# Optimization experiments

Hardware: AMD Instinct MI355X
Metric: run time of the kernel (lower is better)

Reference implementation:

```python
import jax, jax.numpy as jnp
import numpy as np

# Geometry constants fixed by the source's index arithmetic
GRID_P, GRID_Q, NUM_ANCH = 60, 40, 9   # p = (i//9)%60, q = i//(60*9), sr = i%9
N = GRID_P * GRID_Q * NUM_ANCH          # 21600 anchors per image
K = 1000                                # top-K candidates kept before NMS
MAX_BOXES = 18                          # fixed output boxes per image
THRESH = 0.5                            # NMS overlap threshold
BATCH = 64


def setup_inputs() -> dict:
    key = jax.random.key(0)
    k1, k2 = jax.random.split(key)
    x = jax.random.normal(k1, (BATCH, N, 6), dtype=jnp.float32)
    # anchor boxes (x, y, w, h); keep w,h strictly positive and away from 0
    anchor_boxes = jax.random.uniform(k2, (GRID_P, GRID_Q, NUM_ANCH, 4),
                                      dtype=jnp.float32, minval=0.05, maxval=1.0)
    return {"x": x, "anchor_boxes": anchor_boxes}


def _per_sample(ypred, anchors):
    scores, order = jax.lax.top_k(ypred[:, 0], K)          # descending, matches tf.argsort DESC [:1000]
    p = (order // NUM_ANCH) % GRID_P
    q = order // (GRID_P * NUM_ANCH)
    sr = order % NUM_ANCH
    a = anchors[p, q, sr]                                   # [K, 4] (xa, ya, wa, ha)
    regr = ypred[order, 2:6]                                # [K, 4] (dx, dy, dw, dh)
    xc = regr[:, 0] * a[:, 2] + a[:, 0]
    yc = regr[:, 1] * a[:, 3] + a[:, 1]
    w = a[:, 2] * jnp.exp(regr[:, 2])
    h = a[:, 3] * jnp.exp(regr[:, 3])
    cand = jnp.stack([xc, yc, w, h, scores], axis=-1)       # [K, 5] xywh+score

    # xywh -> xyxy for overlap computation (as in non_max_suppression_fast)
    x1 = xc - 0.5 * w; x2 = xc + 0.5 * w
    y1 = yc - 0.5 * h; y2 = yc + 0.5 * h
    area = (x2 - x1) * (y2 - y1)                            # [K]

    # pairwise intersection; overlap[i, j] = inter(i, j) / area(j)  (source divides by
    # the area of the lower-scored candidate, NOT the union -- kept faithfully)
    xx1 = jnp.maximum(x1[:, None], x1[None, :])
    yy1 = jnp.maximum(y1[:, None], y1[None, :])
    xx2 = jnp.minimum(x2[:, None], x2[None, :])
    yy2 = jnp.minimum(y2[:, None], y2[None, :])
    iw = jnp.maximum(0.0, xx2 - xx1)
    ih = jnp.maximum(0.0, yy2 - yy1)
    sup = (iw * ih / area[None, :]) > THRESH                # [K, K] bool

    # greedy NMS over candidates in descending-score order
    jrange = jnp.arange(K)
    def body(i, keep):
        return keep & ~(keep[i] & sup[i] & (jrange > i))
    keep = jax.lax.fori_loop(0, K, body, jnp.ones((K,), dtype=bool))

    # pack first MAX_BOXES kept boxes into fixed-shape output
    ranks = jnp.cumsum(keep) - 1                            # position among kept
    valid = keep & (ranks < MAX_BOXES)
    picked = jnp.zeros((MAX_BOXES, 5), cand.dtype).at[
        jnp.where(valid, ranks, MAX_BOXES)
    ].set(jnp.where(valid[:, None], cand, 0.0), mode='drop')

    # pad with top-scored decoded boxes if fewer than MAX_BOXES survive NMS
    n = jnp.minimum(jnp.sum(keep), MAX_BOXES)
    j = jnp.arange(MAX_BOXES)
    pad = cand[jnp.clip(j - n, 0, K - 1)]
    return jnp.where((j < n)[:, None], picked, pad)         # [MAX_BOXES, 5]


def reference(x, anchor_boxes):
    return jax.vmap(lambda y: _per_sample(y, anchor_boxes))(x)  # [B, 18, 5]
```

## Files before the change

kernel.cpp:

```cpp
#include <hip/hip_runtime.h>

#define NELEM 21600
#define KSEL 1000
#define MAXB 18
#define NT 1024
#define CAP 2048
#define NFULL 21
#define NTAIL (NELEM - NFULL * NT)

typedef unsigned long long ull;

__device__ __forceinline__ unsigned fkey(float f) {
  unsigned u = __float_as_uint(f);
  return (u & 0x80000000u) ? ~u : (u | 0x80000000u);
}
__device__ __forceinline__ float unfkey(unsigned k) {
  unsigned u = (k & 0x80000000u) ? (k ^ 0x80000000u) : ~k;
  return __uint_as_float(u);
}

__device__ void select_bucket(const unsigned* hist, unsigned target,
                              volatile unsigned* chunkSuf,
                              unsigned* outB, unsigned* outCnt, unsigned* outAbove) {
  const int tid = threadIdx.x;
  const int w = tid >> 6, l = tid & 63;
  unsigned h1 = hist[w * 128 + 2 * l + 1];
  unsigned s = hist[w * 128 + 2 * l] + h1;
  #pragma unroll
  for (int d = 1; d < 64; d <<= 1) {
    unsigned t = __shfl_down(s, d);
    if (l + d < 64) s += t;
  }
  if (l == 0) chunkSuf[w] = s;
  __syncthreads();
  if (w == 0) {
    unsigned ct = (l < 16) ? chunkSuf[l] : 0u;
    unsigned cs = ct;
    #pragma unroll
    for (int d = 1; d < 16; d <<= 1) {
      unsigned t = __shfl_down(cs, d);
      if (l + d < 16) cs += t;
    }
    if (l < 16) chunkSuf[l] = cs - ct;
  }
  __syncthreads();
  unsigned base = chunkSuf[w];
  unsigned sufE = s + base;
  unsigned sN = __shfl_down(s, 1);
  unsigned sufN = ((l < 63) ? sN : 0u) + base;
  unsigned geOdd = sufN + h1;
  if (sufE >= target && geOdd < target) { *outB = w * 128u + 2u * l;     *outCnt = sufE;  *outAbove = geOdd; }
  if (geOdd >= target && sufN < target) { *outB = w * 128u + 2u * l + 1; *outCnt = geOdd; *outAbove = sufN;  }
  __syncthreads();
}

__global__ __launch_bounds__(NT, 4) void rpn_kernel(
    const float* __restrict__ x, const float* __restrict__ anch,
    float* __restrict__ out) {
  const int b = blockIdx.x;
  const int tid = threadIdx.x;
  const float* xb = x + (size_t)b * NELEM * 6;

  __shared__ unsigned hist[2048];
  __shared__ unsigned chunkSuf[16];
  __shared__ ull selPk[CAP];
  __shared__ float bX1[KSEL], bY1[KSEL], bX2[KSEL], bY2[KSEL], bAr[KSEL];
  __shared__ unsigned sB, sCnt, sAbove;
  __shared__ unsigned baseKey;
  __shared__ unsigned cnt;
  __shared__ int keptRank[MAXB];
  __shared__ int numKept;

  hist[2 * tid] = 0u; hist[2 * tid + 1] = 0u;

  float sv[NFULL];
  #pragma unroll
  for (int u = 0; u < NFULL; ++u)
    sv[u] = xb[(size_t)(tid + (u << 10)) * 6];
  float stail = 0.f;
  const bool hastail = tid < NTAIL;
  if (hastail) stail = xb[(size_t)(tid + NFULL * NT) * 6];
  asm volatile("" :
      "+v"(sv[0]), "+v"(sv[1]), "+v"(sv[2]), "+v"(sv[3]), "+v"(sv[4]),
      "+v"(sv[5]), "+v"(sv[6]), "+v"(sv[7]), "+v"(sv[8]), "+v"(sv[9]),
      "+v"(sv[10]), "+v"(sv[11]), "+v"(sv[12]), "+v"(sv[13]), "+v"(sv[14]),
      "+v"(sv[15]), "+v"(sv[16]), "+v"(sv[17]), "+v"(sv[18]), "+v"(sv[19]),
      "+v"(sv[20]), "+v"(stail));
  __syncthreads();

  #pragma unroll
  for (int u = 0; u < NFULL; ++u)
    atomicAdd(&hist[fkey(sv[u]) >> 21], 1u);
  if (hastail) atomicAdd(&hist[fkey(stail) >> 21], 1u);
  __syncthreads();
  select_bucket(hist, KSEL, chunkSuf, &sB, &sCnt, &sAbove);
  const unsigned b1 = sB, cnt1 = sCnt, above1 = sAbove;

  if (cnt1 <= CAP) {
    if (tid == 0) { baseKey = b1 << 21; cnt = 0u; }
  } else {
    hist[2 * tid] = 0u; hist[2 * tid + 1] = 0u;
    __syncthreads();
    #pragma unroll
    for (int u = 0; u < NFULL; ++u) {
      unsigned k = fkey(sv[u]);
      if ((k >> 21) == b1) atomicAdd(&hist[(k >> 10) & 0x7FFu], 1u);
    }
    if (hastail) {
      unsigned k = fkey(stail);
      if ((k >> 21) == b1) atomicAdd(&hist[(k >> 10) & 0x7FFu], 1u);
    }
    __syncthreads();
    select_bucket(hist, KSEL - above1, chunkSuf, &sB, &sCnt, &sAbove);
    if (tid == 0) { baseKey = (b1 << 21) | (sB << 10); cnt = 0u; }
  }
  __syncthreads();

  const unsigned TB = baseKey;
  #pragma unroll
  for (int u = 0; u < NFULL; ++u) {
    unsigned k = fkey(sv[u]);
    if (k >= TB) {
      unsigned p = atomicAdd(&cnt, 1u);
      unsigned i = (unsigned)(tid + (u << 10));
      if (p < CAP) selPk[p] = ((ull)k << 32) | (unsigned)(~i);
    }
  }
  if (hastail) {
    unsigned k = fkey(stail);
    if (k >= TB) {
      unsigned p = atomicAdd(&cnt, 1u);
      unsigned i = (unsigned)(tid + NFULL * NT);
      if (p < CAP) selPk[p] = ((ull)k << 32) | (unsigned)(~i);
    }
  }
  __syncthreads();
  const unsigned realCnt = (cnt < CAP) ? cnt : CAP;
  for (unsigned i = realCnt + tid; i < CAP; i += NT) selPk[i] = 0ull;
  __syncthreads();

  {
    const int w = tid >> 6, L = tid & 63;
    const int ea = (w << 7) | (L << 1);
    ull a = selPk[ea], bb = selPk[ea + 1];
    #pragma unroll
    for (unsigned k = 2; k <= 128; k <<= 1) {
      #pragma unroll
      for (unsigned j = k >> 1; j >= 2; j >>= 1) {
        bool up = ((ea & k) == 0);
        bool lower = ((ea & j) == 0);
        bool takeMax = (up == lower);
        ull oa = __shfl_xor(a, (int)(j >> 1));
        ull ob = __shfl_xor(bb, (int)(j >> 1));
        a  = takeMax ? (a  > oa ? a  : oa) : (a  < oa ? a  : oa);
        bb = takeMax ? (bb > ob ? bb : ob) : (bb < ob ? bb : ob);
      }
      bool up = ((ea & k) == 0);
      ull mx = a > bb ? a : bb, mn = a > bb ? bb : a;
      a = up ? mx : mn; bb = up ? mn : mx;
    }
    selPk[ea] = a; selPk[ea + 1] = bb;
    __syncthreads();
    for (unsigned k = 256; k <= 2048; k <<= 1) {
      for (unsigned j = k >> 1; j >= 128; j >>= 1) {
        unsigned p = (unsigned)tid;
        unsigned vi = ((p & ~(j - 1)) << 1) | (p & (j - 1));
        unsigned li = vi | j;
        ull av = selPk[vi], cv = selPk[li];
        bool doswap = ((vi & k) == 0) ? (av < cv) : (av > cv);
        if (doswap) { selPk[vi] = cv; selPk[li] = av; }
        __syncthreads();
      }
      a = selPk[ea]; bb = selPk[ea + 1];
      bool up = (((unsigned)(w << 7) & k) == 0);
      #pragma unroll
      for (unsigned j = 64; j >= 2; j >>= 1) {
        bool lower = ((ea & j) == 0);
        bool takeMax = (up == lower);
        ull oa = __shfl_xor(a, (int)(j >> 1));
        ull ob = __shfl_xor(bb, (int)(j >> 1));
        a  = takeMax ? (a  > oa ? a  : oa) : (a  < oa ? a  : oa);
        bb = takeMax ? (bb > ob ? bb : ob) : (bb < ob ? bb : ob);
      }
      ull mx = a > bb ? a : bb, mn = a > bb ? bb : a;
      a = up ? mx : mn; bb = up ? mn : mx;
      selPk[ea] = a; selPk[ea + 1] = bb;
      __syncthreads();
    }
  }

  if (tid < KSEL) {
    unsigned idx = ~(unsigned)selPk[tid];
    const float2* e2 = (const float2*)(xb + (size_t)idx * 6 + 2);
    float2 ra = e2[0], rb = e2[1];
    unsigned pp = (idx / 9u) % 60u;
    unsigned qq = idx / 540u;
    unsigned sr = idx % 9u;
    const float* ap = anch + (((pp * 40u + qq) * 9u + sr) * 4u);
    float ax = ap[0], ay = ap[1], aw = ap[2], ah = ap[3];
    float xc = ra.x * aw + ax;
    float yc = ra.y * ah + ay;
    float w = aw * expf(rb.x);
    float h = ah * expf(rb.y);
    float x1 = xc - 0.5f * w, x2 = xc + 0.5f * w;
    float y1 = yc - 0.5f * h, y2 = yc + 0.5f * h;
    bX1[tid] = x1; bY1[tid] = y1; bX2[tid] = x2; bY2[tid] = y2;
    bAr[tid] = (x2 - x1) * (y2 - y1);
  }
  __syncthreads();

  if (tid < 64) {
    const int lane = tid;
    int nk = 0;
    float kx1 = 0.f, ky1 = 0.f, kx2 = 0.f, ky2 = 0.f;
    int krank = -1;
    for (int base = 0; base < KSEL && nk < MAXB; base += 64) {
      int c = base + lane;
      bool alive = (c < KSEL);
      int cc = alive ? c : 0;
      float x1 = bX1[cc], y1 = bY1[cc], x2 = bX2[cc], y2 = bY2[cc], ar = bAr[cc];
      for (int i = 0; i < nk; ++i) {
        float px1 = __shfl(kx1, i), py1 = __shfl(ky1, i);
        float px2 = __shfl(kx2, i), py2 = __shfl(ky2, i);
        float iw = fmaxf(fminf(x2, px2) - fmaxf(x1, px1), 0.f);
        float ih = fmaxf(fminf(y2, py2) - fmaxf(y1, py1), 0.f);
        if (iw * ih / ar > 0.5f) alive = false;
      }
      unsigned long long m = __ballot(alive);
      while (m) {
        int i = __builtin_ctzll(m);
        float px1 = __shfl(x1, i), py1 = __shfl(y1, i);
        float px2 = __shfl(x2, i), py2 = __shfl(y2, i);
        if (lane == nk) { kx1 = px1; ky1 = py1; kx2 = px2; ky2 = py2; krank = base + i; }
        ++nk;
        if (nk >= MAXB) break;
        if (alive && lane != i) {
          float iw = fmaxf(fminf(x2, px2) - fmaxf(x1, px1), 0.f);
          float ih = fmaxf(fminf(y2, py2) - fmaxf(y1, py1), 0.f);
          if (iw * ih / ar > 0.5f) alive = false;
        }
        if (lane == i) alive = false;
        m = __ballot(alive);
      }
    }
    if (lane == 0) numKept = nk;
    if (lane < nk) keptRank[lane] = krank;
  }
  __syncthreads();

  const int n = numKept;
  if (tid < MAXB) {
    int j = tid;
    int r = (j < n) ? keptRank[j] : (j - n);
    ull pk = selPk[r];
    unsigned idx = ~(unsigned)pk;
    float sc = unfkey((unsigned)(pk >> 32));
    const float2* e2 = (const float2*)(xb + (size_t)idx * 6 + 2);
    float2 ra = e2[0], rb = e2[1];
    unsigned pp = (idx / 9u) % 60u;
    unsigned qq = idx / 540u;
    unsigned sr = idx % 9u;
    const float* ap = anch + (((pp * 40u + qq) * 9u + sr) * 4u);
    float ax = ap[0], ay = ap[1], aw = ap[2], ah = ap[3];
    float xc = ra.x * aw + ax;
    float yc = ra.y * ah + ay;
    float w = aw * expf(rb.x);
    float h = ah * expf(rb.y);
    float* o = out + b * (MAXB * 5) + j * 5;
    o[0] = xc; o[1] = yc; o[2] = w; o[3] = h; o[4] = sc;
  }
}

extern "C" void kernel_launch(void* const* d_in, const int* in_sizes, int n_in,
                              void* d_out, int out_size, void* d_ws, size_t ws_size,
                              hipStream_t stream) {
  const float* x = (const float*)d_in[0];
  const float* anch = (const float*)d_in[1];
  float* out = (float*)d_out;
  const int B = in_sizes[0] / (NELEM * 6);
  rpn_kernel<<<dim3(B), dim3(NT), 0, stream>>>(x, anch, out);
}
```

Baseline: 63.94 us.

## Split score scan and histogram into a wide pre-pass kernel over chunks

Adds a first kernel that runs four blocks per image. Each block reads a quarter of the objectness scores, converts them to sortable keys, writes the keys compactly to workspace and stores a partial 2048-bin histogram. The select/NMS kernel then sums the partial histograms and reads the contiguous keys instead of the strided 24-byte-stride scores. The aim is to spread the strided load and histogram work across more CUs than the 64 single-block-per-image launch uses. In exchange it adds a second launch plus a workspace round-trip for keys and histograms.

```diff
diff --git a/kernel.cpp b/kernel.cpp
--- a/kernel.cpp
+++ b/kernel.cpp
@@ -5,6 +5,8 @@
 #define MAXB 18
 #define NT 1024
 #define CAP 2048
+#define NCHUNK 4
+#define CHUNK (NELEM / NCHUNK)
 #define NFULL 21
 #define NTAIL (NELEM - NFULL * NT)
 
@@ -17,6 +19,42 @@
 __device__ __forceinline__ float unfkey(unsigned k) {
   unsigned u = (k & 0x80000000u) ? (k ^ 0x80000000u) : ~k;
   return __uint_as_float(u);
+}
+
+__global__ __launch_bounds__(NT) void k1_scan(
+    const float* __restrict__ x, unsigned* __restrict__ gkeys,
+    unsigned* __restrict__ ghist) {
+  const int blk = blockIdx.x;
+  const int s = blk / NCHUNK, c = blk % NCHUNK;
+  const int t = threadIdx.x;
+  const float* xb = x + (size_t)s * NELEM * 6;
+
+  __shared__ unsigned h[2048];
+  h[2 * t] = 0u; h[2 * t + 1] = 0u;
+  __syncthreads();
+
+  const int base = c * CHUNK;
+  unsigned key[6];
+  bool on[6];
+  #pragma unroll
+  for (int k = 0; k < 6; ++k) {
+    int o = t + (k << 10);
+    on[k] = o < CHUNK;
+    int e = base + (on[k] ? o : 0);
+    key[k] = fkey(xb[(size_t)e * 6]);
+  }
+  #pragma unroll
+  for (int k = 0; k < 6; ++k) {
+    if (on[k]) {
+      int e = base + t + (k << 10);
+      gkeys[(size_t)s * NELEM + e] = key[k];
+      atomicAdd(&h[key[k] >> 21], 1u);
+    }
+  }
+  __syncthreads();
+  unsigned* gh = ghist + (size_t)blk * 2048;
+  gh[2 * t] = h[2 * t];
+  gh[2 * t + 1] = h[2 * t + 1];
 }
 
 __device__ void select_bucket(const unsigned* hist, unsigned target,
@@ -54,12 +92,14 @@
   __syncthreads();
 }
 
-__global__ __launch_bounds__(NT, 4) void rpn_kernel(
+__global__ __launch_bounds__(NT, 4) void k2_select(
     const float* __restrict__ x, const float* __restrict__ anch,
+    const unsigned* __restrict__ gkeys, const unsigned* __restrict__ ghist,
     float* __restrict__ out) {
-  const int b = blockIdx.x;
+  const int s = blockIdx.x;
   const int tid = threadIdx.x;
-  const float* xb = x + (size_t)b * NELEM * 6;
+  const float* xb = x + (size_t)s * NELEM * 6;
+  const unsigned* ks = gkeys + (size_t)s * NELEM;
 
   __shared__ unsigned hist[2048];
   __shared__ unsigned chunkSuf[16];
@@ -71,27 +111,29 @@
   __shared__ int keptRank[MAXB];
   __shared__ int numKept;
 
-  hist[2 * tid] = 0u; hist[2 * tid + 1] = 0u;
-
-  float sv[NFULL];
-  #pragma unroll
-  for (int u = 0; u < NFULL; ++u)
-    sv[u] = xb[(size_t)(tid + (u << 10)) * 6];
-  float stail = 0.f;
+  unsigned kv[NFULL];
+  #pragma unroll
+  for (int u = 0; u < NFULL; ++u) kv[u] = ks[tid + (u << 10)];
+  unsigned ktail = 0u;
   const bool hastail = tid < NTAIL;
-  if (hastail) stail = xb[(size_t)(tid + NFULL * NT) * 6];
+  if (hastail) ktail = ks[tid + NFULL * NT];
   asm volatile("" :
-      "+v"(sv[0]), "+v"(sv[1]), "+v"(sv[2]), "+v"(sv[3]), "+v"(sv[4]),
-      "+v"(sv[5]), "+v"(sv[6]), "+v"(sv[7]), "+v"(sv[8]), "+v"(sv[9]),
-      "+v"(sv[10]), "+v"(sv[11]), "+v"(sv[12]), "+v"(sv[13]), "+v"(sv[14]),
-      "+v"(sv[15]), "+v"(sv[16]), "+v"(sv[17]), "+v"(sv[18]), "+v"(sv[19]),
-      "+v"(sv[20]), "+v"(stail));
-  __syncthreads();
-
-  #pragma unroll
-  for (int u = 0; u < NFULL; ++u)
-    atomicAdd(&hist[fkey(sv[u]) >> 21], 1u);
-  if (hastail) atomicAdd(&hist[fkey(stail) >> 21], 1u);
+      "+v"(kv[0]), "+v"(kv[1]), "+v"(kv[2]), "+v"(kv[3]), "+v"(kv[4]),
+      "+v"(kv[5]), "+v"(kv[6]), "+v"(kv[7]), "+v"(kv[8]), "+v"(kv[9]),
+      "+v"(kv[10]), "+v"(kv[11]), "+v"(kv[12]), "+v"(kv[13]), "+v"(kv[14]),
+      "+v"(kv[15]), "+v"(kv[16]), "+v"(kv[17]), "+v"(kv[18]), "+v"(kv[19]),
+      "+v"(kv[20]), "+v"(ktail));
+
+  {
+    unsigned h0 = 0, h1 = 0;
+    #pragma unroll
+    for (int c = 0; c < NCHUNK; ++c) {
+      const unsigned* gh = ghist + (size_t)(s * NCHUNK + c) * 2048;
+      h0 += gh[2 * tid];
+      h1 += gh[2 * tid + 1];
+    }
+    hist[2 * tid] = h0; hist[2 * tid + 1] = h1;
+  }
   __syncthreads();
   select_bucket(hist, KSEL, chunkSuf, &sB, &sCnt, &sAbove);
   const unsigned b1 = sB, cnt1 = sCnt, above1 = sAbove;
@@ -102,14 +144,9 @@
     hist[2 * tid] = 0u; hist[2 * tid + 1] = 0u;
     __syncthreads();
     #pragma unroll
-    for (int u = 0; u < NFULL; ++u) {
-      unsigned k = fkey(sv[u]);
-      if ((k >> 21) == b1) atomicAdd(&hist[(k >> 10) & 0x7FFu], 1u);
-    }
-    if (hastail) {
-      unsigned k = fkey(stail);
-      if ((k >> 21) == b1) atomicAdd(&hist[(k >> 10) & 0x7FFu], 1u);
-    }
+    for (int u = 0; u < NFULL; ++u)
+      if ((kv[u] >> 21) == b1) atomicAdd(&hist[(kv[u] >> 10) & 0x7FFu], 1u);
+    if (hastail && (ktail >> 21) == b1) atomicAdd(&hist[(ktail >> 10) & 0x7FFu], 1u);
     __syncthreads();
     select_bucket(hist, KSEL - above1, chunkSuf, &sB, &sCnt, &sAbove);
     if (tid == 0) { baseKey = (b1 << 21) | (sB << 10); cnt = 0u; }
@@ -119,20 +156,16 @@
   const unsigned TB = baseKey;
   #pragma unroll
   for (int u = 0; u < NFULL; ++u) {
-    unsigned k = fkey(sv[u]);
-    if (k >= TB) {
+    if (kv[u] >= TB) {
       unsigned p = atomicAdd(&cnt, 1u);
       unsigned i = (unsigned)(tid + (u << 10));
-      if (p < CAP) selPk[p] = ((ull)k << 32) | (unsigned)(~i);
-    }
-  }
-  if (hastail) {
-    unsigned k = fkey(stail);
-    if (k >= TB) {
-      unsigned p = atomicAdd(&cnt, 1u);
-      unsigned i = (unsigned)(tid + NFULL * NT);
-      if (p < CAP) selPk[p] = ((ull)k << 32) | (unsigned)(~i);
-    }
+      if (p < CAP) selPk[p] = ((ull)kv[u] << 32) | (unsigned)(~i);
+    }
+  }
+  if (hastail && ktail >= TB) {
+    unsigned p = atomicAdd(&cnt, 1u);
+    unsigned i = (unsigned)(tid + NFULL * NT);
+    if (p < CAP) selPk[p] = ((ull)ktail << 32) | (unsigned)(~i);
   }
   __syncthreads();
   const unsigned realCnt = (cnt < CAP) ? cnt : CAP;
@@ -266,7 +299,7 @@
     float yc = ra.y * ah + ay;
     float w = aw * expf(rb.x);
     float h = ah * expf(rb.y);
-    float* o = out + b * (MAXB * 5) + j * 5;
+    float* o = out + s * (MAXB * 5) + j * 5;
     o[0] = xc; o[1] = yc; o[2] = w; o[3] = h; o[4] = sc;
   }
 }
@@ -278,5 +311,8 @@
   const float* anch = (const float*)d_in[1];
   float* out = (float*)d_out;
   const int B = in_sizes[0] / (NELEM * 6);
-  rpn_kernel<<<dim3(B), dim3(NT), 0, stream>>>(x, anch, out);
-}
+  unsigned* ghist = (unsigned*)d_ws;
+  unsigned* gkeys = ghist + (size_t)B * NCHUNK * 2048;
+  k1_scan<<<dim3(B * NCHUNK), dim3(NT), 0, stream>>>(x, gkeys, ghist);
+  k2_select<<<dim3(B), dim3(NT), 0, stream>>>(x, anch, gkeys, ghist, out);
+}
```

New measurement: 65.66 us. +2.7%, slower.
